# Kernel tuning notes

Hardware: AMD Instinct MI355X
Metric: run time of the kernel (lower is better)

The kernel has to match this reference:

```python
import jax, jax.numpy as jnp
import numpy as np

INPUT_DIM = 128
HIDDEN_DIM = 64
BATCH = 256
SEQ_LEN = 1024


def _projectors(n):
    n_half = n // 2
    S = jnp.zeros((n, n), jnp.float32)
    S = S.at[:n_half, n_half:].set(jnp.eye(n_half))
    S = S.at[n_half:, :n_half].set(jnp.eye(n_half))
    I = jnp.eye(n, dtype=jnp.float32)
    return (I + S) / 2.0, (I - S) / 2.0


def setup_inputs() -> dict:
    key = jax.random.key(0)
    ks = jax.random.split(key, 7)
    x = jax.random.normal(ks[0], (BATCH, SEQ_LEN, INPUT_DIM), jnp.float32)
    A_plus = jax.random.normal(ks[1], (HIDDEN_DIM, HIDDEN_DIM), jnp.float32) * 0.1
    A_minus = jax.random.normal(ks[2], (HIDDEN_DIM, HIDDEN_DIM), jnp.float32) * 0.1
    # nn.Linear default init: U(-1/sqrt(fan_in), 1/sqrt(fan_in))
    b_in = 1.0 / np.sqrt(INPUT_DIM)
    W_in_w = jax.random.uniform(ks[3], (HIDDEN_DIM, INPUT_DIM), jnp.float32, -b_in, b_in)
    W_in_b = jax.random.uniform(ks[4], (HIDDEN_DIM,), jnp.float32, -b_in, b_in)
    b_out = 1.0 / np.sqrt(HIDDEN_DIM)
    W_out_w = jax.random.uniform(ks[5], (INPUT_DIM, HIDDEN_DIM), jnp.float32, -b_out, b_out)
    W_out_b = jax.random.uniform(ks[6], (INPUT_DIM,), jnp.float32, -b_out, b_out)
    bias = jnp.zeros((HIDDEN_DIM,), jnp.float32)
    return {"x": x, "A_plus": A_plus, "A_minus": A_minus,
            "W_in_w": W_in_w, "W_in_b": W_in_b,
            "W_out_w": W_out_w, "W_out_b": W_out_b, "bias": bias}


def reference(x, A_plus, A_minus, W_in_w, W_in_b, W_out_w, W_out_b, bias):
    B, T, _ = x.shape
    H = bias.shape[0]
    P_plus, P_minus = _projectors(H)
    # W_comm = P+ A+ P+ + P- A- P-
    W_comm = P_plus @ A_plus @ P_plus + P_minus @ A_minus @ P_minus
    # Precompute input projection for all timesteps (one big GEMM): (B,T,H)
    inp = jnp.einsum('bti,hi->bth', x, W_in_w) + W_in_b + bias
    inp_t = jnp.transpose(inp, (1, 0, 2))  # (T,B,H)

    def step(h, u_t):
        h = jnp.tanh(h @ W_comm.T + u_t)
        return h, None

    h0 = jnp.zeros((B, H), x.dtype)
    hidden, _ = jax.lax.scan(step, h0, inp_t)
    predictions = hidden @ W_out_w.T + W_out_b  # (B, input_dim)
    return predictions, hidden
```

## Files before the change

kernel.cpp:

```cpp
#include <hip/hip_runtime.h>
#include <hip/hip_bf16.h>

#define BB 256
#define TT 1024
#define II 128
#define HH 64

#define PRESCALE 2.8853900817779268f

typedef float    f32x4_t __attribute__((ext_vector_type(4)));
typedef _Float16 h16x2   __attribute__((ext_vector_type(2)));
typedef _Float16 h16x4   __attribute__((ext_vector_type(4)));
typedef _Float16 h16x8   __attribute__((ext_vector_type(8)));
typedef __fp16   p16x2   __attribute__((ext_vector_type(2)));

union UH2 { unsigned u; h16x2 h; p16x2 p; };
union U4H8 { uint4 u; h16x8 h; };
union B128 { uint4 u; h16x2 h[4]; };

__device__ __forceinline__ float tanh_pre(float a){
  float e = __builtin_amdgcn_exp2f(a);
  return __builtin_fmaf(-2.0f, __builtin_amdgcn_rcpf(1.0f + e), 1.0f);
}

#if __has_builtin(__builtin_amdgcn_fdot2)
__device__ __forceinline__ float fdot2f(h16x2 a, h16x2 b, float c){
  return __builtin_amdgcn_fdot2(a, b, c, false);
}
#else
__device__ __forceinline__ float fdot2f(h16x2 a, h16x2 b, float c){
  return __builtin_fmaf((float)a[1], (float)b[1], __builtin_fmaf((float)a[0], (float)b[0], c));
}
#endif

#if __has_builtin(__builtin_amdgcn_permlane32_swap)
__device__ __forceinline__ float half_swap(float v){
  unsigned vu = __float_as_uint(v);
  auto r = __builtin_amdgcn_permlane32_swap(vu, vu, false, false);
  return __uint_as_float(((unsigned)r[0]) ^ ((unsigned)r[1]) ^ vu);
}
#else
__device__ __forceinline__ float half_swap(float v){
  return __shfl_xor(v, 32, 64);
}
#endif

__global__ void k_prep(const float* __restrict__ Ap, const float* __restrict__ Am,
                       const float* __restrict__ Winw,
                       const float* __restrict__ Winb, const float* __restrict__ bias,
                       float* __restrict__ wsf, unsigned* __restrict__ whf,
                       unsigned short* __restrict__ wsb){
  const int tid = threadIdx.x;
  if (tid < 64) wsf[4096 + tid] = (Winb[tid] + bias[tid]) * PRESCALE;
  for (int e = tid; e < 1024; e += 256){
    int lane = e >> 4, jp = e & 15, row = lane & 31, j = 2*jp;
    float v0, v1;
    if (lane < 32){
      v0 = 0.25f*PRESCALE*(Ap[row*64+j]     + Ap[row*64+j+32]     + Ap[(row+32)*64+j]     + Ap[(row+32)*64+j+32]);
      v1 = 0.25f*PRESCALE*(Ap[row*64+j+1]   + Ap[row*64+j+33]     + Ap[(row+32)*64+j+1]   + Ap[(row+32)*64+j+33]);
    } else {
      v0 = 0.25f*PRESCALE*(Am[row*64+j]     - Am[row*64+j+32]     - Am[(row+32)*64+j]     + Am[(row+32)*64+j+32]);
      v1 = 0.25f*PRESCALE*(Am[row*64+j+1]   - Am[row*64+j+33]     - Am[(row+32)*64+j+1]   + Am[(row+32)*64+j+33]);
    }
    UH2 p;
    p.h[0] = (_Float16)v0;
    p.h[1] = (_Float16)v1;
    whf[e] = p.u;
  }
  for (int e = tid; e < 8192; e += 256){
    int j = e & 7, lane = (e >> 3) & 63, fidx = e >> 9;
    int ks = fidx >> 2, nt = fidx & 3, l15 = lane & 15, q = lane >> 4;
    union { _Float16 f; unsigned short s; } cv;
    cv.f = (_Float16)(Winw[(nt*16 + l15)*II + ks*32 + q*8 + j] * PRESCALE);
    wsb[e] = cv.s;
  }
}

__global__ __launch_bounds__(256, 1) void k_fused(const float* __restrict__ x,
                                                  const float* __restrict__ wsf,
                                                  const unsigned* __restrict__ whf,
                                                  const unsigned short* __restrict__ wsb,
                                                  const float* __restrict__ Wout,
                                                  const float* __restrict__ Woutb,
                                                  float* __restrict__ out){
  extern __shared__ unsigned char smem[];
  unsigned short* Us    = (unsigned short*)smem;
  unsigned*       flags = (unsigned*)(smem + 131072);
  unsigned*       Hb    = (unsigned*)(smem + 131072 + 256);

  const int b    = blockIdx.x;
  const int tid  = threadIdx.x;
  const int lane = tid & 63;
  const int wave = tid >> 6;
  const int l15  = lane & 15;
  const int q    = lane >> 4;

  if (tid < 64) flags[tid] = 0u;
  __syncthreads();

  if (wave != 0){
    h16x8 bfr[4][4];
    #pragma unroll
    for (int ks = 0; ks < 4; ++ks)
      #pragma unroll
      for (int nt = 0; nt < 4; ++nt)
        bfr[ks][nt] = *(const h16x8*)(wsb + ((ks*4 + nt)*64 + lane)*8);

    float bcv[4];
    #pragma unroll
    for (int nt = 0; nt < 4; ++nt) bcv[nt] = wsf[4096 + nt*16 + l15];

    const float* xb = x + (long)b * (TT * II);

    #pragma unroll 1
    for (int tile = wave - 1; tile < 64; tile += 3){
      const int trow = tile * 16;
      const float* xa = xb + (trow + l15) * II + q*8;
      h16x8 afr[4];
      #pragma unroll
      for (int ks = 0; ks < 4; ++ks){
        float4 a0 = *(const float4*)(xa + ks*32);
        float4 a1 = *(const float4*)(xa + ks*32 + 4);
        U4H8 v;
        UH2 p0, p1, p2, p3;
        p0.p = __builtin_amdgcn_cvt_pkrtz(a0.x, a0.y);
        p1.p = __builtin_amdgcn_cvt_pkrtz(a0.z, a0.w);
        p2.p = __builtin_amdgcn_cvt_pkrtz(a1.x, a1.y);
        p3.p = __builtin_amdgcn_cvt_pkrtz(a1.z, a1.w);
        v.u.x = p0.u; v.u.y = p1.u; v.u.z = p2.u; v.u.w = p3.u;
        afr[ks] = v.h;
      }
      f32x4_t acc[4];
      #pragma unroll
      for (int nt = 0; nt < 4; ++nt){
        acc[nt][0]=bcv[nt]; acc[nt][1]=bcv[nt]; acc[nt][2]=bcv[nt]; acc[nt][3]=bcv[nt];
      }
      #pragma unroll
      for (int ks = 0; ks < 4; ++ks){
        #pragma unroll
        for (int nt = 0; nt < 4; ++nt){
          acc[nt] = __builtin_amdgcn_mfma_f32_16x16x32_f16(afr[ks], bfr[ks][nt], acc[nt], 0, 0, 0);
        }
      }
      const int tg = tile*4 + q;
      #pragma unroll
      for (int nt = 0; nt < 4; ++nt){
        UH2 lo, hi;
        lo.p = __builtin_amdgcn_cvt_pkrtz(acc[nt][0], acc[nt][1]);
        hi.p = __builtin_amdgcn_cvt_pkrtz(acc[nt][2], acc[nt][3]);
        uint2 pk; pk.x = lo.u; pk.y = hi.u;
        *(uint2*)&Us[(tg*64 + nt*16 + l15) * 4] = pk;
      }
      __threadfence_block();
      if (lane == 0)
        __hip_atomic_store(&flags[tile], 1u, __ATOMIC_RELEASE, __HIP_MEMORY_SCOPE_WORKGROUP);
    }
    return;
  }

  h16x2 w[16];
  {
    const uint4* wr = (const uint4*)(whf + lane * 16);
    #pragma unroll
    for (int j4 = 0; j4 < 4; ++j4){
      uint4 v = wr[j4];
      UH2 c0, c1, c2, c3;
      c0.u = v.x; c1.u = v.y; c2.u = v.z; c3.u = v.w;
      w[4*j4+0] = c0.h; w[4*j4+1] = c1.h; w[4*j4+2] = c2.h; w[4*j4+3] = c3.h;
    }
  }

  const bool  lo    = (lane < 32);
  const float sgn   = lo ? 1.0f : -1.0f;
  const int   hslot = (lane >> 1) + (lane & 1) * 32;
  const uint4* Hr   = (const uint4*)((const unsigned char*)Hb + (lane & 32) * 2);

  while (!__hip_atomic_load(&flags[0], __ATOMIC_ACQUIRE, __HIP_MEMORY_SCOPE_WORKGROUP)) {}

  const h16x4* Ul = (const h16x4*)Us;
  h16x4 uc = Ul[0*64 + lane];
  h16x4 u1 = Ul[1*64 + lane];

  float h = 0.0f;
  int last_ready = 0;
  #pragma unroll 1
  for (int tile = 0; tile < 64; ++tile){
    int wt = tile + 1; if (wt > 63) wt = 63;
    if (wt > last_ready){
      while (!__hip_atomic_load(&flags[wt], __ATOMIC_ACQUIRE, __HIP_MEMORY_SCOPE_WORKGROUP)) {}
      last_ready = wt;
    }
    #pragma unroll
    for (int tgl = 0; tgl < 4; ++tgl){
      const int tg = tile*4 + tgl;
      int tp = tg + 2; if (tp > TT/4 - 1) tp = TT/4 - 1;
      h16x4 u2 = Ul[tp*64 + lane];
      float ug0 = (float)uc[0], ug1 = (float)uc[1], ug2 = (float)uc[2], ug3 = (float)uc[3];
      #pragma unroll
      for (int g = 0; g < 4; ++g){
        float ugv = (g==0) ? ug0 : (g==1) ? ug1 : (g==2) ? ug2 : ug3;
        float hsw = half_swap(h);
        float sd  = __builtin_fmaf(h, sgn, hsw);
        unsigned nbu = (unsigned)__builtin_amdgcn_mov_dpp(__float_as_uint(sd), 0xB1, 0xF, 0xF, true);
        UH2 hp; hp.p = __builtin_amdgcn_cvt_pkrtz(sd, __uint_as_float(nbu));
        Hb[hslot] = hp.u;
        __asm__ volatile("" ::: "memory");
        __builtin_amdgcn_sched_barrier(0);
        B128 hv[4];
        #pragma unroll
        for (int r = 0; r < 4; ++r) hv[r].u = Hr[r];
        float a0 = 0.0f, a1 = 0.0f, a2 = 0.0f, a3 = 0.0f;
        #pragma unroll
        for (int jp = 0; jp < 16; jp += 4){
          a0 = fdot2f(w[jp+0], hv[(jp+0)>>2].h[(jp+0)&3], a0);
          a1 = fdot2f(w[jp+1], hv[(jp+1)>>2].h[(jp+1)&3], a1);
          a2 = fdot2f(w[jp+2], hv[(jp+2)>>2].h[(jp+2)&3], a2);
          a3 = fdot2f(w[jp+3], hv[(jp+3)>>2].h[(jp+3)&3], a3);
        }
        float z = (a0 + a1) + (a2 + a3);
        float zsw = half_swap(z);
        float a = __builtin_fmaf(z, sgn, zsw) + ugv;
        h = tanh_pre(a);
      }
      uc = u1; u1 = u2;
    }
  }

  unsigned hu = __float_as_uint(h);
  float p0 = Woutb[lane];
  float p1 = Woutb[lane + 64];
  #pragma unroll 8
  for (int j = 0; j < 64; ++j){
    float hj = __uint_as_float(__builtin_amdgcn_readlane(hu, j));
    p0 = __builtin_fmaf(Wout[lane * HH + j],        hj, p0);
    p1 = __builtin_fmaf(Wout[(lane + 64) * HH + j], hj, p1);
  }
  out[b * 128 + lane]           = p0;
  out[b * 128 + 64 + lane]      = p1;
  out[BB * 128 + b * 64 + lane] = h;
}

extern "C" void kernel_launch(void* const* d_in, const int* in_sizes, int n_in,
                              void* d_out, int out_size, void* d_ws, size_t ws_size,
                              hipStream_t stream){
  const float* x     = (const float*)d_in[0];
  const float* Ap    = (const float*)d_in[1];
  const float* Am    = (const float*)d_in[2];
  const float* Winw  = (const float*)d_in[3];
  const float* Winb  = (const float*)d_in[4];
  const float* Woutw = (const float*)d_in[5];
  const float* Woutb = (const float*)d_in[6];
  const float* bias  = (const float*)d_in[7];

  float*          wsf = (float*)d_ws;
  unsigned*       whf = (unsigned*)((char*)d_ws + 16640);
  unsigned short* wsb = (unsigned short*)((char*)d_ws + 24832);

  float* out = (float*)d_out;

  hipFuncSetAttribute((const void*)k_fused,
                      hipFuncAttributeMaxDynamicSharedMemorySize, 131584);

  hipLaunchKernelGGL(k_prep,  dim3(1),   dim3(256), 0,      stream, Ap, Am, Winw, Winb, bias, wsf, whf, wsb);
  hipLaunchKernelGGL(k_fused, dim3(BB),  dim3(256), 131584, stream, x, wsf, whf, wsb, Woutw, Woutb, out);
}
```

Measured before the change: 311.4 us.

## Carry sigmoid-form state r instead of tanh to shorten recurrent critical path

The recurrence now keeps r = 1/(1+e) rather than h = 1-2r. The affine term is folded into the weights (scaled by -2) and into a per-row bias built from the A_plus row sums, so each step drops an FMA on the serial chain. The per-step h exchange also changes: each lane writes one fp16 value directly, which removes the DPP neighbour move and the packed convert, and the matvec loop is reindexed. Rounding may change slightly because the constant part is now carried in fp32 bias while the fp16 weights are doubled.

```diff
diff --git a/kernel.cpp b/kernel.cpp
--- a/kernel.cpp
+++ b/kernel.cpp
@@ -18,11 +18,6 @@
 union U4H8 { uint4 u; h16x8 h; };
 union B128 { uint4 u; h16x2 h[4]; };
 
-__device__ __forceinline__ float tanh_pre(float a){
-  float e = __builtin_amdgcn_exp2f(a);
-  return __builtin_fmaf(-2.0f, __builtin_amdgcn_rcpf(1.0f + e), 1.0f);
-}
-
 #if __has_builtin(__builtin_amdgcn_fdot2)
 __device__ __forceinline__ float fdot2f(h16x2 a, h16x2 b, float c){
   return __builtin_amdgcn_fdot2(a, b, c, false);
@@ -33,17 +28,19 @@
 }
 #endif
 
+__device__ __forceinline__ void half_pair(float v, float& blo, float& bhi){
 #if __has_builtin(__builtin_amdgcn_permlane32_swap)
-__device__ __forceinline__ float half_swap(float v){
   unsigned vu = __float_as_uint(v);
   auto r = __builtin_amdgcn_permlane32_swap(vu, vu, false, false);
-  return __uint_as_float(((unsigned)r[0]) ^ ((unsigned)r[1]) ^ vu);
-}
+  blo = __uint_as_float((unsigned)r[0]);
+  bhi = __uint_as_float((unsigned)r[1]);
 #else
-__device__ __forceinline__ float half_swap(float v){
-  return __shfl_xor(v, 32, 64);
-}
+  float sw = __shfl_xor(v, 32, 64);
+  bool lo = ((threadIdx.x & 63) < 32);
+  blo = lo ? v : sw;
+  bhi = lo ? sw : v;
 #endif
+}
 
 __global__ void k_prep(const float* __restrict__ Ap, const float* __restrict__ Am,
                        const float* __restrict__ Winw,
@@ -51,16 +48,21 @@
                        float* __restrict__ wsf, unsigned* __restrict__ whf,
                        unsigned short* __restrict__ wsb){
   const int tid = threadIdx.x;
-  if (tid < 64) wsf[4096 + tid] = (Winb[tid] + bias[tid]) * PRESCALE;
+  if (tid < 64){
+    int row = tid & 31;
+    float cs = 0.0f;
+    for (int j = 0; j < 64; ++j) cs += Ap[row*64 + j] + Ap[(row+32)*64 + j];
+    wsf[4096 + tid] = (Winb[tid] + bias[tid]) * PRESCALE + 0.5f * PRESCALE * cs;
+  }
   for (int e = tid; e < 1024; e += 256){
     int lane = e >> 4, jp = e & 15, row = lane & 31, j = 2*jp;
     float v0, v1;
     if (lane < 32){
-      v0 = 0.25f*PRESCALE*(Ap[row*64+j]     + Ap[row*64+j+32]     + Ap[(row+32)*64+j]     + Ap[(row+32)*64+j+32]);
-      v1 = 0.25f*PRESCALE*(Ap[row*64+j+1]   + Ap[row*64+j+33]     + Ap[(row+32)*64+j+1]   + Ap[(row+32)*64+j+33]);
+      v0 = -0.5f*PRESCALE*(Ap[row*64+j]   + Ap[row*64+j+32] + Ap[(row+32)*64+j]   + Ap[(row+32)*64+j+32]);
+      v1 = -0.5f*PRESCALE*(Ap[row*64+j+1] + Ap[row*64+j+33] + Ap[(row+32)*64+j+1] + Ap[(row+32)*64+j+33]);
     } else {
-      v0 = 0.25f*PRESCALE*(Am[row*64+j]     - Am[row*64+j+32]     - Am[(row+32)*64+j]     + Am[(row+32)*64+j+32]);
-      v1 = 0.25f*PRESCALE*(Am[row*64+j+1]   - Am[row*64+j+33]     - Am[(row+32)*64+j+1]   + Am[(row+32)*64+j+33]);
+      v0 = -0.5f*PRESCALE*(Am[row*64+j]   - Am[row*64+j+32] - Am[(row+32)*64+j]   + Am[(row+32)*64+j+32]);
+      v1 = -0.5f*PRESCALE*(Am[row*64+j+1] - Am[row*64+j+33] - Am[(row+32)*64+j+1] + Am[(row+32)*64+j+33]);
     }
     UH2 p;
     p.h[0] = (_Float16)v0;
@@ -86,7 +88,7 @@
   extern __shared__ unsigned char smem[];
   unsigned short* Us    = (unsigned short*)smem;
   unsigned*       flags = (unsigned*)(smem + 131072);
-  unsigned*       Hb    = (unsigned*)(smem + 131072 + 256);
+  unsigned short* Hw    = (unsigned short*)(smem + 131072 + 256);
 
   const int b    = blockIdx.x;
   const int tid  = threadIdx.x;
@@ -170,10 +172,9 @@
     }
   }
 
-  const bool  lo    = (lane < 32);
-  const float sgn   = lo ? 1.0f : -1.0f;
-  const int   hslot = (lane >> 1) + (lane & 1) * 32;
-  const uint4* Hr   = (const uint4*)((const unsigned char*)Hb + (lane & 32) * 2);
+  const bool  lo  = (lane < 32);
+  const float sgn = lo ? 1.0f : -1.0f;
+  const uint4* Hr = (const uint4*)((const unsigned char*)Hw + (lane & 32) * 2);
 
   while (!__hip_atomic_load(&flags[0], __ATOMIC_ACQUIRE, __HIP_MEMORY_SCOPE_WORKGROUP)) {}
 
@@ -181,7 +182,7 @@
   h16x4 uc = Ul[0*64 + lane];
   h16x4 u1 = Ul[1*64 + lane];
 
-  float h = 0.0f;
+  float r = 0.5f;
   int last_ready = 0;
   #pragma unroll 1
   for (int tile = 0; tile < 64; ++tile){
@@ -199,33 +200,36 @@
       #pragma unroll
       for (int g = 0; g < 4; ++g){
         float ugv = (g==0) ? ug0 : (g==1) ? ug1 : (g==2) ? ug2 : ug3;
-        float hsw = half_swap(h);
-        float sd  = __builtin_fmaf(h, sgn, hsw);
-        unsigned nbu = (unsigned)__builtin_amdgcn_mov_dpp(__float_as_uint(sd), 0xB1, 0xF, 0xF, true);
-        UH2 hp; hp.p = __builtin_amdgcn_cvt_pkrtz(sd, __uint_as_float(nbu));
-        Hb[hslot] = hp.u;
+        float r0, r1;
+        half_pair(r, r0, r1);
+        float val = __builtin_fmaf(r1, sgn, r0);
+        _Float16 vh = (_Float16)val;
+        Hw[lane] = *(unsigned short*)&vh;
         __asm__ volatile("" ::: "memory");
         __builtin_amdgcn_sched_barrier(0);
         B128 hv[4];
         #pragma unroll
-        for (int r = 0; r < 4; ++r) hv[r].u = Hr[r];
+        for (int rr = 0; rr < 4; ++rr) hv[rr].u = Hr[rr];
         float a0 = 0.0f, a1 = 0.0f, a2 = 0.0f, a3 = 0.0f;
         #pragma unroll
-        for (int jp = 0; jp < 16; jp += 4){
-          a0 = fdot2f(w[jp+0], hv[(jp+0)>>2].h[(jp+0)&3], a0);
-          a1 = fdot2f(w[jp+1], hv[(jp+1)>>2].h[(jp+1)&3], a1);
-          a2 = fdot2f(w[jp+2], hv[(jp+2)>>2].h[(jp+2)&3], a2);
-          a3 = fdot2f(w[jp+3], hv[(jp+3)>>2].h[(jp+3)&3], a3);
+        for (int jp = 0; jp < 4; ++jp){
+          a0 = fdot2f(w[jp+ 0], hv[0].h[jp], a0);
+          a1 = fdot2f(w[jp+ 4], hv[1].h[jp], a1);
+          a2 = fdot2f(w[jp+ 8], hv[2].h[jp], a2);
+          a3 = fdot2f(w[jp+12], hv[3].h[jp], a3);
         }
-        float z = (a0 + a1) + (a2 + a3);
-        float zsw = half_swap(z);
-        float a = __builtin_fmaf(z, sgn, zsw) + ugv;
-        h = tanh_pre(a);
+        float y = (a0 + a1) + (a2 + a3);
+        float y0, y1;
+        half_pair(y, y0, y1);
+        float a = __builtin_fmaf(y1, sgn, y0) + ugv;
+        float e = __builtin_amdgcn_exp2f(a);
+        r = __builtin_amdgcn_rcpf(1.0f + e);
       }
       uc = u1; u1 = u2;
     }
   }
 
+  float h = __builtin_fmaf(-2.0f, r, 1.0f);
   unsigned hu = __float_as_uint(h);
   float p0 = Woutb[lane];
   float p1 = Woutb[lane + 64];
@@ -259,8 +263,8 @@
   float* out = (float*)d_out;
 
   hipFuncSetAttribute((const void*)k_fused,
-                      hipFuncAttributeMaxDynamicSharedMemorySize, 131584);
+                      hipFuncAttributeMaxDynamicSharedMemorySize, 131456);
 
   hipLaunchKernelGGL(k_prep,  dim3(1),   dim3(256), 0,      stream, Ap, Am, Winw, Winb, bias, wsf, whf, wsb);
-  hipLaunchKernelGGL(k_fused, dim3(BB),  dim3(256), 131584, stream, x, wsf, whf, wsb, Woutw, Woutb, out);
-}
+  hipLaunchKernelGGL(k_fused, dim3(BB),  dim3(256), 131456, stream, x, wsf, whf, wsb, Woutw, Woutb, out);
+}
```

Result: faster. 292.1 us (-6.2%).
